# Kernel optimization log

Measured on AMD Instinct MI355X. Metric: run time of the kernel, lower is better.

## Reference

```python
import jax, jax.numpy as jnp
import numpy as np

B, N, E = 16, 5000, 40000
IN_DIM, HID, GRU_OUT = 128, 512, 16
G0, G1, G2 = 1, 128, 128          # gcn_dim = [1,128,128]
M0, M1, M2 = 512, 1024, N * GRU_OUT  # gru_out_linear MLP dims (hidden_num prepended)
EPS = 1e-5                         # BatchNorm1d eps (eval: running mean 0, var 1)


def _gcn_norm(edge_index, n):
    loop = jnp.arange(n)
    src = jnp.concatenate([edge_index[0], loop])
    dst = jnp.concatenate([edge_index[1], loop])
    deg = jax.ops.segment_sum(jnp.ones(src.shape[0], jnp.float32), dst, num_segments=n)
    dinv = 1.0 / jnp.sqrt(deg)
    return src, dst, dinv[src] * dinv[dst]


def _gcn_conv(h, W, b, src, dst, norm):
    hw = jnp.einsum('bnf,fg->bng', h, W)
    msgs = hw[:, src, :] * norm[None, :, None]            # [B,E+N,Fout]
    agg = jax.ops.segment_sum(jnp.swapaxes(msgs, 0, 1), dst, num_segments=h.shape[1])
    return jnp.swapaxes(agg, 0, 1) + b


def _gru_cell(x, h, Wih, Whh, bih, bhh):
    gi = x @ Wih.T + bih
    gh = h @ Whh.T + bhh
    ir, iz, ig = jnp.split(gi, 3, axis=-1)
    hr, hz, hg = jnp.split(gh, 3, axis=-1)
    r = jax.nn.sigmoid(ir + hr)
    z = jax.nn.sigmoid(iz + hz)
    n = jnp.tanh(ig + r * hg)
    return (1.0 - z) * n + z * h


def _mlp_block(x, W, b, a, g, be):
    # Dropout(eval)=Identity -> Linear -> PReLU -> BatchNorm1d(eval, rm=0, rv=1)
    y = x @ W.T + b
    y = jnp.where(y >= 0, y, a * y)
    return y / jnp.sqrt(1.0 + EPS) * g + be


def setup_inputs():
    key = jax.random.key(0)
    ks = jax.random.split(key, 32)
    f = lambda i, shp, s=0.02: jax.random.normal(ks[i], shp, jnp.float32) * s
    return dict(
        x=jax.random.normal(ks[0], (B, IN_DIM), jnp.float32),
        smoothed_vert_pos=jax.random.normal(ks[1], (B, N * 3), jnp.float32),
        edge_index=jax.random.randint(ks[2], (2, E), 0, N),
        Wih=f(3, (3 * HID, IN_DIM)), Whh=f(4, (3 * HID, HID)),
        bih=f(5, (3 * HID,)), bhh=f(6, (3 * HID,)),
        Wg1=f(7, (G0, G1), 0.1), bg1=f(8, (G1,)),
        Wg2=f(9, (G1, G2), 0.1), bg2=f(10, (G2,)),
        W1=f(11, (M1, M0)), b1=f(12, (M1,)),
        a1=jnp.full((M1,), 0.25, jnp.float32),
        g1=1.0 + f(13, (M1,)), be1=f(14, (M1,)),
        W2=f(15, (M2, M1), 0.01), b2=f(16, (M2,)),
        a2=jnp.full((M2,), 0.25, jnp.float32),
        g2=1.0 + f(17, (M2,)), be2=f(18, (M2,)),
        Wo=f(19, (1, G2 + GRU_OUT)), bo=f(20, (1,)),
    )


def reference(x, smoothed_vert_pos, edge_index, Wih, Whh, bih, bhh,
              Wg1, bg1, Wg2, bg2, W1, b1, a1, g1, be1,
              W2, b2, a2, g2, be2, Wo, bo):
    b = x.shape[0]
    svp = smoothed_vert_pos.reshape(b, N, 3)
    src, dst, norm = _gcn_norm(edge_index, N)
    z = svp[:, :, 2:3]                                   # channel j+2, j=0
    h1 = _gcn_conv(z, Wg1, bg1, src, dst, norm)          # [B,N,G1], no nonlinearity between convs (as in source)
    res = _gcn_conv(h1, Wg2, bg2, src, dst, norm)        # [B,N,G2]
    hidden = jnp.zeros((b, HID), x.dtype)                # hidden=None path
    next_hidden = _gru_cell(x, hidden, Wih, Whh, bih, bhh)
    m = _mlp_block(next_hidden, W1, b1, a1, g1, be1)
    m = _mlp_block(m, W2, b2, a2, g2, be2)
    gru_out = m.reshape(b, N, GRU_OUT)
    y = jnp.concatenate([gru_out, res], axis=2) @ Wo.T + bo  # [B,N,1]
    return y.reshape(b, N), next_hidden
```

## Files before the change

### kernel.cpp

```cpp
#include <hip/hip_runtime.h>
#include <hip/hip_bf16.h>

#define NN 5000
#define BB 16
#define EE 40000
#define INF 128
#define HID 512
#define M1D 1024
#define EPSV 1e-5f

typedef float f4 __attribute__((ext_vector_type(4)));

__device__ __forceinline__ float dot4(f4 a, f4 b) {
    return fmaf(a.x, b.x, fmaf(a.y, b.y, fmaf(a.z, b.z, a.w * b.w)));
}
__device__ __forceinline__ f4 ntload(const float* p) {
    return __builtin_nontemporal_load((const f4*)p);
}
__device__ __forceinline__ float dpp_xor1(float x) {
    return __int_as_float(__builtin_amdgcn_update_dpp(0, __float_as_int(x), 0xB1, 0xF, 0xF, true));
}
__device__ __forceinline__ float dpp_xor2(float x) {
    return __int_as_float(__builtin_amdgcn_update_dpp(0, __float_as_int(x), 0x4E, 0xF, 0xF, true));
}
__device__ __forceinline__ float dpp_xor8(float x) {
    return __int_as_float(__builtin_amdgcn_update_dpp(0, __float_as_int(x), 0x128, 0xF, 0xF, true));
}

#define GRU_BLOCKS 128
#define DEG_BLOCKS 157
#define ZPACK_BLOCKS 313
#define ZERO_BLOCKS 157

__global__ __launch_bounds__(256)
void k_s1(const int* __restrict__ ei, const float* __restrict__ x,
          const float* __restrict__ svp,
          const float* __restrict__ Wih, const float* __restrict__ bih,
          const float* __restrict__ bhh,
          const float* __restrict__ Wg1, const float* __restrict__ bg1,
          const float* __restrict__ Wg2, const float* __restrict__ bg2,
          const float* __restrict__ Wo, const float* __restrict__ bo,
          float* __restrict__ deg, float* __restrict__ nh,
          float* __restrict__ outNH, float* __restrict__ cst,
          float* __restrict__ zpack, float* __restrict__ zerobase) {
    const int blk = blockIdx.x;
    const int tid = threadIdx.x;

    if (blk < GRU_BLOCKS) {
        const int t = blk * 256 + tid;
        const int q = t & 3, idx = t >> 2;
        const int b = idx >> 9, h = idx & 511;
        const float* xb = x + b * INF;
        const float* wr = Wih + (size_t)h * INF;
        const float* wz = Wih + (size_t)(HID + h) * INF;
        const float* wg = Wih + (size_t)(2 * HID + h) * INF;
        float ir = 0.f, iz = 0.f, ig = 0.f;
        #pragma unroll 8
        for (int i = 0; i < 8; ++i) {
            const int k0 = i * 16 + q * 4;
            const f4 xv = *(const f4*)(xb + k0);
            ir += dot4(xv, *(const f4*)(wr + k0));
            iz += dot4(xv, *(const f4*)(wz + k0));
            ig += dot4(xv, *(const f4*)(wg + k0));
        }
        ir += __shfl_xor(ir, 1); ir += __shfl_xor(ir, 2);
        iz += __shfl_xor(iz, 1); iz += __shfl_xor(iz, 2);
        ig += __shfl_xor(ig, 1); ig += __shfl_xor(ig, 2);
        if (q == 0) {
            ir += bih[h]; iz += bih[HID + h]; ig += bih[2 * HID + h];
            float r  = 1.f / (1.f + expf(-(ir + bhh[h])));
            float z  = 1.f / (1.f + expf(-(iz + bhh[HID + h])));
            float nv = tanhf(ig + r * bhh[2 * HID + h]);
            float v  = (1.f - z) * nv;
            nh[idx] = v;
            outNH[idx] = v;
        }
    } else if (blk < GRU_BLOCKS + DEG_BLOCKS) {
        const int e = (blk - GRU_BLOCKS) * 256 + tid;
        if (e < EE) atomicAdd(&deg[ei[EE + e]], 1.0f);
    } else if (blk == GRU_BLOCKS + DEG_BLOCKS) {
        __shared__ float su[128], sv[128], sc[128];
        const int g = tid;
        if (g < 128) {
            float t = 0.f;
            for (int c = 0; c < 128; ++c) t = fmaf(Wg2[g * 128 + c], Wo[16 + c], t);
            su[g] = Wg1[g] * t;
            sv[g] = bg1[g] * t;
            sc[g] = bg2[g] * Wo[16 + g];
        }
        __syncthreads();
        for (int s = 64; s > 0; s >>= 1) {
            if (g < s) { su[g] += su[g + s]; sv[g] += sv[g + s]; sc[g] += sc[g + s]; }
            __syncthreads();
        }
        if (g == 0) { cst[0] = su[0]; cst[1] = sv[0]; cst[2] = sc[0] + bo[0]; }
    } else if (blk < GRU_BLOCKS + DEG_BLOCKS + 1 + ZPACK_BLOCKS) {
        const int t = (blk - (GRU_BLOCKS + DEG_BLOCKS + 1)) * 256 + tid;
        if (t < NN * BB) {
            const int n = t >> 4, b = t & 15;
            zpack[t] = svp[b * (NN * 3) + 3 * n + 2];
        }
    } else {
        const int t = (blk - (GRU_BLOCKS + DEG_BLOCKS + 1 + ZPACK_BLOCKS)) * 256 + tid;
        if (t < 2 * BB * NN / 4) ((f4*)zerobase)[t] = (f4)(0.f);
    }
}

#define MLP_BLOCKS 256
#define AGG1_BLOCKS 744
#define AGG1_PER_BLOCK 861

__global__ __launch_bounds__(256)
void k_s2(const int* __restrict__ ei, const float* __restrict__ deg,
          const float* __restrict__ zpack, const float* __restrict__ nh,
          const float* __restrict__ W1, const float* __restrict__ b1,
          const float* __restrict__ a1, const float* __restrict__ g1,
          const float* __restrict__ be1,
          float* __restrict__ m1, float* __restrict__ aggzE, float* __restrict__ s1E) {
    const int blk = blockIdx.x;
    const int tid = threadIdx.x;

    if (blk < MLP_BLOCKS) {
        const int t = blk * 256 + tid;
        const int q = t & 3, idx = t >> 2;
        const int b = idx >> 10, i = idx & 1023;
        const float* hb = nh + b * HID;
        const float* wr = W1 + (size_t)i * HID;
        float acc = 0.f;
        #pragma unroll 8
        for (int ii = 0; ii < 32; ++ii) {
            const int k0 = ii * 16 + q * 4;
            acc += dot4(*(const f4*)(hb + k0), *(const f4*)(wr + k0));
        }
        acc += __shfl_xor(acc, 1); acc += __shfl_xor(acc, 2);
        if (q == 0) {
            acc += b1[i];
            float v = acc >= 0.f ? acc : a1[i] * acc;
            m1[idx] = v * (1.f / sqrtf(1.f + EPSV)) * g1[i] + be1[i];
        }
    } else {
        const int base = (blk - MLP_BLOCKS) * AGG1_PER_BLOCK;
        #pragma unroll
        for (int i = 0; i < 4; ++i) {
            const int it = i * 256 + tid;
            if (it < AGG1_PER_BLOCK) {
                const int t = base + it;
                if (t < EE * BB) {
                    const int e = t >> 4, b = t & 15;
                    const int s = ei[e], d = ei[EE + e];
                    const float w = rsqrtf(1.f + deg[s]) * rsqrtf(1.f + deg[d]);
                    atomicAdd(&aggzE[d * 16 + b], w * zpack[s * 16 + b]);
                    if (b == 0) atomicAdd(&s1E[d], w);
                }
            }
        }
    }
}

#define BIG_BLOCKS 1000
#define AGG2_PER_BLOCK 640

__global__ __launch_bounds__(256, 4)
void k_s3(const float* __restrict__ W2, const float* __restrict__ m1,
          const float* __restrict__ b2, const float* __restrict__ a2,
          const float* __restrict__ g2, const float* __restrict__ be2,
          const float* __restrict__ Wo,
          const int* __restrict__ ei, const float* __restrict__ deg,
          const float* __restrict__ zpack, const float* __restrict__ aggzE,
          float* __restrict__ aggz2E, float* __restrict__ ysum) {
    __shared__ float accs[4][80][16];
    const int blk = blockIdx.x;
    const int tid = threadIdx.x;

    {
        const int base = blk * AGG2_PER_BLOCK;
        #pragma unroll
        for (int i = 0; i < 3; ++i) {
            const int it = i * 256 + tid;
            if (it < AGG2_PER_BLOCK) {
                const int t = base + it;
                const int e = t >> 4, b = t & 15;
                const int s = ei[e], d = ei[EE + e];
                const float degs = deg[s];
                const float d2s = 1.f / (1.f + degs);
                const float w = rsqrtf(1.f + degs) * rsqrtf(1.f + deg[d]);
                const float A1s = aggzE[s * 16 + b] + d2s * zpack[s * 16 + b];
                atomicAdd(&aggz2E[d * 16 + b], w * A1s);
            }
        }
    }

    const int w = tid >> 6, l = tid & 63;
    const int koff = w * 256 + l * 4;
    const int n0 = blk * 5;
    const int jbase = n0 * 16;

    float4 m1r[16];
    #pragma unroll
    for (int b = 0; b < 16; ++b)
        m1r[b] = *(const float4*)(m1 + b * M1D + koff);

    const int hi0 = l & 1, hi1 = (l >> 1) & 1, hi2 = (l >> 2) & 1, hi3 = (l >> 3) & 1;
    const int brev = ((l & 1) << 3) | ((l & 2) << 1) | ((l & 4) >> 1) | ((l & 8) >> 3);

    const float* wp = W2 + (size_t)jbase * M1D + koff;
    f4 w0 = ntload(wp);
    f4 w1 = ntload(wp + M1D);
    f4 w2v = ntload(wp + 2 * M1D);
    for (int jj = 0; jj < 80; ++jj) {
        const int jn = (jj + 3 < 80) ? (jj + 3) : 79;
        const f4 wn = ntload(wp + (size_t)jn * M1D);
        float acc[16];
        #pragma unroll
        for (int b = 0; b < 16; ++b)
            acc[b] = fmaf(w0.x, m1r[b].x, fmaf(w0.y, m1r[b].y,
                     fmaf(w0.z, m1r[b].z, w0.w * m1r[b].w)));
        float r8[8];
        #pragma unroll
        for (int i = 0; i < 8; ++i) {
            float keep = hi0 ? acc[8 + i] : acc[i];
            float send = hi0 ? acc[i]     : acc[8 + i];
            r8[i] = keep + dpp_xor1(send);
        }
        float r4[4];
        #pragma unroll
        for (int i = 0; i < 4; ++i) {
            float keep = hi1 ? r8[4 + i] : r8[i];
            float send = hi1 ? r8[i]     : r8[4 + i];
            r4[i] = keep + dpp_xor2(send);
        }
        float r2[2];
        #pragma unroll
        for (int i = 0; i < 2; ++i) {
            float keep = hi2 ? r4[2 + i] : r4[i];
            float send = hi2 ? r4[i]     : r4[2 + i];
            r2[i] = keep + __shfl_xor(send, 4, 64);
        }
        float keep = hi3 ? r2[1] : r2[0];
        float send = hi3 ? r2[0] : r2[1];
        float r1 = keep + dpp_xor8(send);
        r1 += __shfl_xor(r1, 16, 64);
        r1 += __shfl_xor(r1, 32, 64);
        if (l < 16) accs[w][jj][brev] = r1;
        w0 = w1; w1 = w2v; w2v = wn;
    }
    __syncthreads();

    if (tid < 80) {
        const int nl = tid >> 4, b = tid & 15;
        const float invs = 1.f / sqrtf(1.f + EPSV);
        float sum = 0.f;
        #pragma unroll
        for (int kk = 0; kk < 16; ++kk) {
            const int rloc = nl * 16 + kk;
            const int j = jbase + rloc;
            float a = accs[0][rloc][b] + accs[1][rloc][b]
                    + accs[2][rloc][b] + accs[3][rloc][b] + b2[j];
            float v = a >= 0.f ? a : a2[j] * a;
            float val = v * invs * g2[j] + be2[j];
            sum = fmaf(val, Wo[kk], sum);
        }
        ysum[n0 * 16 + tid] = sum;
    }
}

__global__ __launch_bounds__(256)
void k_fin(const float* __restrict__ ysum, const float* __restrict__ aggzE,
           const float* __restrict__ aggz2E, const float* __restrict__ s1E,
           const float* __restrict__ deg, const float* __restrict__ zpack,
           const float* __restrict__ cst, float* __restrict__ y) {
    const int t = blockIdx.x * 256 + threadIdx.x;
    if (t >= BB * NN) return;
    const int n = t >> 4, b = t & 15;
    const float U = cst[0], V = cst[1], C0 = cst[2];
    const float d2 = 1.f / (1.f + deg[n]);
    const float z  = zpack[t];
    const float A1 = aggzE[t] + d2 * z;
    const float A2 = aggz2E[t] + d2 * A1;
    const float S1v = s1E[n] + d2;
    y[b * NN + n] = ysum[t] + U * A2 + V * S1v + C0;
}


extern "C" void kernel_launch(void* const* d_in, const int* in_sizes, int n_in,
                              void* d_out, int out_size, void* d_ws, size_t ws_size,
                              hipStream_t stream) {
    const float* x   = (const float*)d_in[0];
    const float* svp = (const float*)d_in[1];
    const int*   ei  = (const int*)d_in[2];
    const float* Wih = (const float*)d_in[3];
    const float* bih = (const float*)d_in[5];
    const float* bhh = (const float*)d_in[6];
    const float* Wg1 = (const float*)d_in[7];
    const float* bg1 = (const float*)d_in[8];
    const float* Wg2 = (const float*)d_in[9];
    const float* bg2 = (const float*)d_in[10];
    const float* W1  = (const float*)d_in[11];
    const float* b1  = (const float*)d_in[12];
    const float* a1  = (const float*)d_in[13];
    const float* g1  = (const float*)d_in[14];
    const float* be1 = (const float*)d_in[15];
    const float* W2  = (const float*)d_in[16];
    const float* b2  = (const float*)d_in[17];
    const float* a2  = (const float*)d_in[18];
    const float* g2  = (const float*)d_in[19];
    const float* be2 = (const float*)d_in[20];
    const float* Wo  = (const float*)d_in[21];
    const float* bo  = (const float*)d_in[22];
    float* out = (float*)d_out;

    float* ws      = (float*)d_ws;
    float* deg     = ws;
    float* s1E     = deg + NN;
    float* aggzE   = s1E + NN;
    float* aggz2E  = aggzE + BB * NN;
    float* zpack   = aggz2E + BB * NN;
    float* ysum    = zpack + BB * NN;
    float* nh      = ysum + BB * NN;
    float* m1      = nh + BB * HID;
    float* cst     = m1 + BB * M1D;

    hipMemsetAsync(ws, 0, (size_t)(2 * NN) * sizeof(float), stream);

    k_s1<<<dim3(GRU_BLOCKS + DEG_BLOCKS + 1 + ZPACK_BLOCKS + ZERO_BLOCKS),
           dim3(256), 0, stream>>>(
        ei, x, svp, Wih, bih, bhh, Wg1, bg1, Wg2, bg2, Wo, bo,
        deg, nh, out + BB * NN, cst, zpack, aggzE );

    k_s2<<<dim3(MLP_BLOCKS + AGG1_BLOCKS), dim3(256), 0, stream>>>(
        ei, deg, zpack, nh, W1, b1, a1, g1, be1, m1, aggzE, s1E);

    k_s3<<<dim3(BIG_BLOCKS), dim3(256), 0, stream>>>(
        W2, m1, b2, a2, g2, be2, Wo, ei, deg, zpack, aggzE, aggz2E, ysum);

    k_fin<<<dim3((BB * NN + 255) / 256), dim3(256), 0, stream>>>(
        ysum, aggzE, aggz2E, s1E, deg, zpack, cst, out);
}
```

Before: 107.9 us.

## Fuse stage-2, stage-3 and finalize kernels into one cooperative kernel with grid syncs

Replaces three separate launches (MLP1/agg1, agg2/W2 stream, finalize) with one cooperative kernel of 1000 blocks that uses grid.sync between phases. The aim is to remove kernel launch gaps and tail effects between the dependent stages. The fused kernel needs all 1000 blocks resident at once (256 CUs at 4 blocks each), and grid syncs add their own barrier cost. If the cooperative launch fails, the code falls back to the old three-kernel path.

```diff
diff --git a/kernel.cpp b/kernel.cpp
--- a/kernel.cpp
+++ b/kernel.cpp
@@ -1,5 +1,8 @@
 #include <hip/hip_runtime.h>
 #include <hip/hip_bf16.h>
+#include <hip/hip_cooperative_groups.h>
+
+namespace cg = cooperative_groups;
 
 #define NN 5000
 #define BB 16
@@ -25,6 +28,140 @@
 }
 __device__ __forceinline__ float dpp_xor8(float x) {
     return __int_as_float(__builtin_amdgcn_update_dpp(0, __float_as_int(x), 0x128, 0xF, 0xF, true));
+}
+
+
+__device__ __forceinline__ void mlp_body(int blk, int tid, const float* nh,
+        const float* W1, const float* b1, const float* a1, const float* g1,
+        const float* be1, float* m1) {
+    const int t = blk * 256 + tid;
+    const int q = t & 3, idx = t >> 2;
+    const int b = idx >> 10, i = idx & 1023;
+    const float* hb = nh + b * HID;
+    const float* wr = W1 + (size_t)i * HID;
+    float acc = 0.f;
+    #pragma unroll 8
+    for (int ii = 0; ii < 32; ++ii) {
+        const int k0 = ii * 16 + q * 4;
+        acc += dot4(*(const f4*)(hb + k0), *(const f4*)(wr + k0));
+    }
+    acc += __shfl_xor(acc, 1); acc += __shfl_xor(acc, 2);
+    if (q == 0) {
+        acc += b1[i];
+        float v = acc >= 0.f ? acc : a1[i] * acc;
+        m1[idx] = v * (1.f / sqrtf(1.f + EPSV)) * g1[i] + be1[i];
+    }
+}
+
+__device__ __forceinline__ void agg1_item(int t, const int* ei, const float* deg,
+        const float* zpack, float* aggzE, float* s1E) {
+    const int e = t >> 4, b = t & 15;
+    const int s = ei[e], d = ei[EE + e];
+    const float w = rsqrtf(1.f + deg[s]) * rsqrtf(1.f + deg[d]);
+    atomicAdd(&aggzE[d * 16 + b], w * zpack[s * 16 + b]);
+    if (b == 0) atomicAdd(&s1E[d], w);
+}
+
+__device__ __forceinline__ void agg2_item(int t, const int* ei, const float* deg,
+        const float* zpack, const float* aggzE, float* aggz2E) {
+    const int e = t >> 4, b = t & 15;
+    const int s = ei[e], d = ei[EE + e];
+    const float degs = deg[s];
+    const float d2s = 1.f / (1.f + degs);
+    const float w = rsqrtf(1.f + degs) * rsqrtf(1.f + deg[d]);
+    const float A1s = aggzE[s * 16 + b] + d2s * zpack[s * 16 + b];
+    atomicAdd(&aggz2E[d * 16 + b], w * A1s);
+}
+
+__device__ __forceinline__ void stream_body(int blk, int tid,
+        float (*accs)[80][16],
+        const float* W2, const float* m1, const float* b2, const float* a2,
+        const float* g2, const float* be2, const float* Wo, float* ysum) {
+    const int w = tid >> 6, l = tid & 63;
+    const int koff = w * 256 + l * 4;
+    const int n0 = blk * 5;
+    const int jbase = n0 * 16;
+
+    float4 m1r[16];
+    #pragma unroll
+    for (int b = 0; b < 16; ++b)
+        m1r[b] = *(const float4*)(m1 + b * M1D + koff);
+
+    const int hi0 = l & 1, hi1 = (l >> 1) & 1, hi2 = (l >> 2) & 1, hi3 = (l >> 3) & 1;
+    const int brev = ((l & 1) << 3) | ((l & 2) << 1) | ((l & 4) >> 1) | ((l & 8) >> 3);
+
+    const float* wp = W2 + (size_t)jbase * M1D + koff;
+    f4 w0 = ntload(wp);
+    f4 w1 = ntload(wp + M1D);
+    f4 w2v = ntload(wp + 2 * M1D);
+    for (int jj = 0; jj < 80; ++jj) {
+        const int jn = (jj + 3 < 80) ? (jj + 3) : 79;
+        const f4 wn = ntload(wp + (size_t)jn * M1D);
+        float acc[16];
+        #pragma unroll
+        for (int b = 0; b < 16; ++b)
+            acc[b] = fmaf(w0.x, m1r[b].x, fmaf(w0.y, m1r[b].y,
+                     fmaf(w0.z, m1r[b].z, w0.w * m1r[b].w)));
+        float r8[8];
+        #pragma unroll
+        for (int i = 0; i < 8; ++i) {
+            float keep = hi0 ? acc[8 + i] : acc[i];
+            float send = hi0 ? acc[i]     : acc[8 + i];
+            r8[i] = keep + dpp_xor1(send);
+        }
+        float r4[4];
+        #pragma unroll
+        for (int i = 0; i < 4; ++i) {
+            float keep = hi1 ? r8[4 + i] : r8[i];
+            float send = hi1 ? r8[i]     : r8[4 + i];
+            r4[i] = keep + dpp_xor2(send);
+        }
+        float r2[2];
+        #pragma unroll
+        for (int i = 0; i < 2; ++i) {
+            float keep = hi2 ? r4[2 + i] : r4[i];
+            float send = hi2 ? r4[i]     : r4[2 + i];
+            r2[i] = keep + __shfl_xor(send, 4, 64);
+        }
+        float keep = hi3 ? r2[1] : r2[0];
+        float send = hi3 ? r2[0] : r2[1];
+        float r1 = keep + dpp_xor8(send);
+        r1 += __shfl_xor(r1, 16, 64);
+        r1 += __shfl_xor(r1, 32, 64);
+        if (l < 16) accs[w][jj][brev] = r1;
+        w0 = w1; w1 = w2v; w2v = wn;
+    }
+    __syncthreads();
+
+    if (tid < 80) {
+        const int nl = tid >> 4, b = tid & 15;
+        const float invs = 1.f / sqrtf(1.f + EPSV);
+        float sum = 0.f;
+        #pragma unroll
+        for (int kk = 0; kk < 16; ++kk) {
+            const int rloc = nl * 16 + kk;
+            const int j = jbase + rloc;
+            float a = accs[0][rloc][b] + accs[1][rloc][b]
+                    + accs[2][rloc][b] + accs[3][rloc][b] + b2[j];
+            float v = a >= 0.f ? a : a2[j] * a;
+            float val = v * invs * g2[j] + be2[j];
+            sum = fmaf(val, Wo[kk], sum);
+        }
+        ysum[n0 * 16 + tid] = sum;
+    }
+}
+
+__device__ __forceinline__ void fin_item(int t, const float* ysum,
+        const float* aggzE, const float* aggz2E, const float* s1E,
+        const float* deg, const float* zpack, const float* cst, float* y) {
+    const int n = t >> 4, b = t & 15;
+    const float U = cst[0], V = cst[1], C0 = cst[2];
+    const float d2 = 1.f / (1.f + deg[n]);
+    const float z  = zpack[t];
+    const float A1 = aggzE[t] + d2 * z;
+    const float A2 = aggz2E[t] + d2 * A1;
+    const float S1v = s1E[n] + d2;
+    y[b * NN + n] = ysum[t] + U * A2 + V * S1v + C0;
 }
 
 #define GRU_BLOCKS 128
@@ -106,9 +243,61 @@
     }
 }
 
+#define COOP_BLOCKS 1000
 #define MLP_BLOCKS 256
 #define AGG1_BLOCKS 744
 #define AGG1_PER_BLOCK 861
+#define AGG2_PER_BLOCK 640
+
+__global__ __launch_bounds__(256, 4)
+void k_coop(const float* __restrict__ W2, float* m1,
+            const float* __restrict__ b2, const float* __restrict__ a2,
+            const float* __restrict__ g2, const float* __restrict__ be2,
+            const float* __restrict__ Wo,
+            const int* __restrict__ ei, const float* __restrict__ deg,
+            const float* __restrict__ zpack, float* aggzE,
+            float* aggz2E, float* s1E, float* ysum,
+            const float* __restrict__ nh,
+            const float* __restrict__ W1, const float* __restrict__ b1,
+            const float* __restrict__ a1, const float* __restrict__ g1,
+            const float* __restrict__ be1,
+            const float* __restrict__ cst, float* __restrict__ y) {
+    cg::grid_group grid = cg::this_grid();
+    __shared__ float accs[4][80][16];
+    const int blk = blockIdx.x;
+    const int tid = threadIdx.x;
+
+    if (blk < MLP_BLOCKS) {
+        mlp_body(blk, tid, nh, W1, b1, a1, g1, be1, m1);
+    } else {
+        const int base = (blk - MLP_BLOCKS) * AGG1_PER_BLOCK;
+        #pragma unroll
+        for (int i = 0; i < 4; ++i) {
+            const int it = i * 256 + tid;
+            if (it < AGG1_PER_BLOCK) {
+                const int t = base + it;
+                if (t < EE * BB) agg1_item(t, ei, deg, zpack, aggzE, s1E);
+            }
+        }
+    }
+
+    grid.sync();
+
+    {
+        const int base = blk * AGG2_PER_BLOCK;
+        #pragma unroll
+        for (int i = 0; i < 3; ++i) {
+            const int it = i * 256 + tid;
+            if (it < AGG2_PER_BLOCK) agg2_item(base + it, ei, deg, zpack, aggzE, aggz2E);
+        }
+    }
+    stream_body(blk, tid, accs, W2, m1, b2, a2, g2, be2, Wo, ysum);
+
+    grid.sync();
+
+    if (tid < 80) fin_item(blk * 80 + tid, ysum, aggzE, aggz2E, s1E, deg, zpack, cst, y);
+}
+
 
 __global__ __launch_bounds__(256)
 void k_s2(const int* __restrict__ ei, const float* __restrict__ deg,
@@ -116,28 +305,11 @@
           const float* __restrict__ W1, const float* __restrict__ b1,
           const float* __restrict__ a1, const float* __restrict__ g1,
           const float* __restrict__ be1,
-          float* __restrict__ m1, float* __restrict__ aggzE, float* __restrict__ s1E) {
+          float* m1, float* aggzE, float* s1E) {
     const int blk = blockIdx.x;
     const int tid = threadIdx.x;
-
     if (blk < MLP_BLOCKS) {
-        const int t = blk * 256 + tid;
-        const int q = t & 3, idx = t >> 2;
-        const int b = idx >> 10, i = idx & 1023;
-        const float* hb = nh + b * HID;
-        const float* wr = W1 + (size_t)i * HID;
-        float acc = 0.f;
-        #pragma unroll 8
-        for (int ii = 0; ii < 32; ++ii) {
-            const int k0 = ii * 16 + q * 4;
-            acc += dot4(*(const f4*)(hb + k0), *(const f4*)(wr + k0));
-        }
-        acc += __shfl_xor(acc, 1); acc += __shfl_xor(acc, 2);
-        if (q == 0) {
-            acc += b1[i];
-            float v = acc >= 0.f ? acc : a1[i] * acc;
-            m1[idx] = v * (1.f / sqrtf(1.f + EPSV)) * g1[i] + be1[i];
-        }
+        mlp_body(blk, tid, nh, W1, b1, a1, g1, be1, m1);
     } else {
         const int base = (blk - MLP_BLOCKS) * AGG1_PER_BLOCK;
         #pragma unroll
@@ -145,20 +317,11 @@
             const int it = i * 256 + tid;
             if (it < AGG1_PER_BLOCK) {
                 const int t = base + it;
-                if (t < EE * BB) {
-                    const int e = t >> 4, b = t & 15;
-                    const int s = ei[e], d = ei[EE + e];
-                    const float w = rsqrtf(1.f + deg[s]) * rsqrtf(1.f + deg[d]);
-                    atomicAdd(&aggzE[d * 16 + b], w * zpack[s * 16 + b]);
-                    if (b == 0) atomicAdd(&s1E[d], w);
-                }
+                if (t < EE * BB) agg1_item(t, ei, deg, zpack, aggzE, s1E);
             }
         }
     }
 }
-
-#define BIG_BLOCKS 1000
-#define AGG2_PER_BLOCK 640
 
 __global__ __launch_bounds__(256, 4)
 void k_s3(const float* __restrict__ W2, const float* __restrict__ m1,
@@ -167,101 +330,19 @@
           const float* __restrict__ Wo,
           const int* __restrict__ ei, const float* __restrict__ deg,
           const float* __restrict__ zpack, const float* __restrict__ aggzE,
-          float* __restrict__ aggz2E, float* __restrict__ ysum) {
+          float* aggz2E, float* ysum) {
     __shared__ float accs[4][80][16];
     const int blk = blockIdx.x;
     const int tid = threadIdx.x;
-
     {
         const int base = blk * AGG2_PER_BLOCK;
         #pragma unroll
         for (int i = 0; i < 3; ++i) {
             const int it = i * 256 + tid;
-            if (it < AGG2_PER_BLOCK) {
-                const int t = base + it;
-                const int e = t >> 4, b = t & 15;
-                const int s = ei[e], d = ei[EE + e];
-                const float degs = deg[s];
-                const float d2s = 1.f / (1.f + degs);
-                const float w = rsqrtf(1.f + degs) * rsqrtf(1.f + deg[d]);
-                const float A1s = aggzE[s * 16 + b] + d2s * zpack[s * 16 + b];
-                atomicAdd(&aggz2E[d * 16 + b], w * A1s);
-            }
-        }
-    }
-
-    const int w = tid >> 6, l = tid & 63;
-    const int koff = w * 256 + l * 4;
-    const int n0 = blk * 5;
-    const int jbase = n0 * 16;
-
-    float4 m1r[16];
-    #pragma unroll
-    for (int b = 0; b < 16; ++b)
-        m1r[b] = *(const float4*)(m1 + b * M1D + koff);
-
-    const int hi0 = l & 1, hi1 = (l >> 1) & 1, hi2 = (l >> 2) & 1, hi3 = (l >> 3) & 1;
-    const int brev = ((l & 1) << 3) | ((l & 2) << 1) | ((l & 4) >> 1) | ((l & 8) >> 3);
-
-    const float* wp = W2 + (size_t)jbase * M1D + koff;
-    f4 w0 = ntload(wp);
-    f4 w1 = ntload(wp + M1D);
-    f4 w2v = ntload(wp + 2 * M1D);
-    for (int jj = 0; jj < 80; ++jj) {
-        const int jn = (jj + 3 < 80) ? (jj + 3) : 79;
-        const f4 wn = ntload(wp + (size_t)jn * M1D);
-        float acc[16];
-        #pragma unroll
-        for (int b = 0; b < 16; ++b)
-            acc[b] = fmaf(w0.x, m1r[b].x, fmaf(w0.y, m1r[b].y,
-                     fmaf(w0.z, m1r[b].z, w0.w * m1r[b].w)));
-        float r8[8];
-        #pragma unroll
-        for (int i = 0; i < 8; ++i) {
-            float keep = hi0 ? acc[8 + i] : acc[i];
-            float send = hi0 ? acc[i]     : acc[8 + i];
-            r8[i] = keep + dpp_xor1(send);
-        }
-        float r4[4];
-        #pragma unroll
-        for (int i = 0; i < 4; ++i) {
-            float keep = hi1 ? r8[4 + i] : r8[i];
-            float send = hi1 ? r8[i]     : r8[4 + i];
-            r4[i] = keep + dpp_xor2(send);
-        }
-        float r2[2];
-        #pragma unroll
-        for (int i = 0; i < 2; ++i) {
-            float keep = hi2 ? r4[2 + i] : r4[i];
-            float send = hi2 ? r4[i]     : r4[2 + i];
-            r2[i] = keep + __shfl_xor(send, 4, 64);
-        }
-        float keep = hi3 ? r2[1] : r2[0];
-        float send = hi3 ? r2[0] : r2[1];
-        float r1 = keep + dpp_xor8(send);
-        r1 += __shfl_xor(r1, 16, 64);
-        r1 += __shfl_xor(r1, 32, 64);
-        if (l < 16) accs[w][jj][brev] = r1;
-        w0 = w1; w1 = w2v; w2v = wn;
-    }
-    __syncthreads();
-
-    if (tid < 80) {
-        const int nl = tid >> 4, b = tid & 15;
-        const float invs = 1.f / sqrtf(1.f + EPSV);
-        float sum = 0.f;
-        #pragma unroll
-        for (int kk = 0; kk < 16; ++kk) {
-            const int rloc = nl * 16 + kk;
-            const int j = jbase + rloc;
-            float a = accs[0][rloc][b] + accs[1][rloc][b]
-                    + accs[2][rloc][b] + accs[3][rloc][b] + b2[j];
-            float v = a >= 0.f ? a : a2[j] * a;
-            float val = v * invs * g2[j] + be2[j];
-            sum = fmaf(val, Wo[kk], sum);
-        }
-        ysum[n0 * 16 + tid] = sum;
-    }
+            if (it < AGG2_PER_BLOCK) agg2_item(base + it, ei, deg, zpack, aggzE, aggz2E);
+        }
+    }
+    stream_body(blk, tid, accs, W2, m1, b2, a2, g2, be2, Wo, ysum);
 }
 
 __global__ __launch_bounds__(256)
@@ -270,15 +351,7 @@
            const float* __restrict__ deg, const float* __restrict__ zpack,
            const float* __restrict__ cst, float* __restrict__ y) {
     const int t = blockIdx.x * 256 + threadIdx.x;
-    if (t >= BB * NN) return;
-    const int n = t >> 4, b = t & 15;
-    const float U = cst[0], V = cst[1], C0 = cst[2];
-    const float d2 = 1.f / (1.f + deg[n]);
-    const float z  = zpack[t];
-    const float A1 = aggzE[t] + d2 * z;
-    const float A2 = aggz2E[t] + d2 * A1;
-    const float S1v = s1E[n] + d2;
-    y[b * NN + n] = ysum[t] + U * A2 + V * S1v + C0;
+    if (t < BB * NN) fin_item(t, ysum, aggzE, aggz2E, s1E, deg, zpack, cst, y);
 }
 
 
@@ -322,17 +395,26 @@
 
     hipMemsetAsync(ws, 0, (size_t)(2 * NN) * sizeof(float), stream);
 
+    float* outNH = out + BB * NN;
     k_s1<<<dim3(GRU_BLOCKS + DEG_BLOCKS + 1 + ZPACK_BLOCKS + ZERO_BLOCKS),
            dim3(256), 0, stream>>>(
         ei, x, svp, Wih, bih, bhh, Wg1, bg1, Wg2, bg2, Wo, bo,
-        deg, nh, out + BB * NN, cst, zpack, aggzE );
-
-    k_s2<<<dim3(MLP_BLOCKS + AGG1_BLOCKS), dim3(256), 0, stream>>>(
-        ei, deg, zpack, nh, W1, b1, a1, g1, be1, m1, aggzE, s1E);
-
-    k_s3<<<dim3(BIG_BLOCKS), dim3(256), 0, stream>>>(
-        W2, m1, b2, a2, g2, be2, Wo, ei, deg, zpack, aggzE, aggz2E, ysum);
-
-    k_fin<<<dim3((BB * NN + 255) / 256), dim3(256), 0, stream>>>(
-        ysum, aggzE, aggz2E, s1E, deg, zpack, cst, out);
-}
+        deg, nh, outNH, cst, zpack, aggzE );
+
+    void* args[] = {
+        (void*)&W2, (void*)&m1, (void*)&b2, (void*)&a2, (void*)&g2, (void*)&be2,
+        (void*)&Wo, (void*)&ei, (void*)&deg, (void*)&zpack, (void*)&aggzE,
+        (void*)&aggz2E, (void*)&s1E, (void*)&ysum, (void*)&nh, (void*)&W1,
+        (void*)&b1, (void*)&a1, (void*)&g1, (void*)&be1, (void*)&cst, (void*)&out
+    };
+    hipError_t cerr = hipLaunchCooperativeKernel((const void*)k_coop,
+                          dim3(COOP_BLOCKS), dim3(256), args, 0, stream);
+    if (cerr != hipSuccess) {
+        k_s2<<<dim3(MLP_BLOCKS + AGG1_BLOCKS), dim3(256), 0, stream>>>(
+            ei, deg, zpack, nh, W1, b1, a1, g1, be1, m1, aggzE, s1E);
+        k_s3<<<dim3(COOP_BLOCKS), dim3(256), 0, stream>>>(
+            W2, m1, b2, a2, g2, be2, Wo, ei, deg, zpack, aggzE, aggz2E, ysum);
+        k_fin<<<dim3((BB * NN + 255) / 256), dim3(256), 0, stream>>>(
+            ysum, aggzE, aggz2E, s1E, deg, zpack, cst, out);
+    }
+}
```

Measured after the change: 344.4 us. 219% more time.
